# Kernel tuning notes

Measured on AMD Instinct MI355X. Metric: run time of the kernel, lower is better.

Reference implementation:

```python
import jax, jax.numpy as jnp
import numpy as np

SEQ, D_IN, D_OUT = 4096, 1024, 1024


def setup_inputs() -> dict:
    key = jax.random.key(0)
    k_emb, k_q, k_k, k_v = jax.random.split(key, 4)
    # torch Linear stores weight as [out, in]; we keep [in, out] for x @ W
    scale = 1.0 / np.sqrt(D_IN)
    return {
        "embeddings": jax.random.normal(k_emb, (SEQ, D_IN), dtype=jnp.float32),
        "w_query": jax.random.uniform(k_q, (D_IN, D_OUT), dtype=jnp.float32, minval=-scale, maxval=scale),
        "w_key": jax.random.uniform(k_k, (D_IN, D_OUT), dtype=jnp.float32, minval=-scale, maxval=scale),
        "w_value": jax.random.uniform(k_v, (D_IN, D_OUT), dtype=jnp.float32, minval=-scale, maxval=scale),
    }


def reference(embeddings, w_query, w_key, w_value):
    # QKV projections (bias=False)
    q = embeddings @ w_query  # [S, D_out]
    k = embeddings @ w_key    # [S, D_out]
    v = embeddings @ w_value  # [S, D_out]
    inv_sqrt_d = 1.0 / jnp.sqrt(jnp.asarray(k.shape[-1], dtype=q.dtype))
    scores = jnp.einsum("sd,td->st", q, k) * inv_sqrt_d  # [S, S]
    weights = jax.nn.softmax(scores, axis=-1)
    return weights @ v  # [S, D_out]
```

## Files before the change

### kernel.cpp

```cpp
#include <hip/hip_runtime.h>
#include <hip/hip_bf16.h>

typedef unsigned short u16;
typedef __bf16 bf16x8 __attribute__((ext_vector_type(8)));
typedef float f32x4 __attribute__((ext_vector_type(4)));
typedef unsigned short u16x8 __attribute__((ext_vector_type(8)));
typedef unsigned short u16x4 __attribute__((ext_vector_type(4)));

__device__ __forceinline__ float bf2f(u16 u) {
  unsigned x = ((unsigned)u) << 16;
  return __builtin_bit_cast(float, x);
}
__device__ __forceinline__ u16 f2bf(float f) {
  unsigned u = __builtin_bit_cast(unsigned, f);
  u += 0x7fffu + ((u >> 16) & 1u);
  return (u16)(u >> 16);
}

__device__ __forceinline__ void gload16(const u16* g, u16* lds) {
  __builtin_amdgcn_global_load_lds(
      (const __attribute__((address_space(1))) void*)g,
      (__attribute__((address_space(3))) void*)lds,
      16, 0, 0);
}

template <int OUT_MODE, int NX, int BK>
__device__ __forceinline__ void gemm_body(
    const u16* __restrict__ A, int lda,
    const u16* __restrict__ B, int ldb,
    void* __restrict__ C, int ldc, int K, float cscale)
{
  __shared__ __align__(16) u16 As[128 * BK];
  __shared__ __align__(16) u16 Bs[128 * BK];

  constexpr int CPR = BK / 8;
  constexpr int RPG = 512 / BK;
  constexpr int IPW = 32 / RPG;

  const int b = blockIdx.x;
  const int by = (b & 7) + 8 * (b / (8 * NX));
  const int bx = (b >> 3) % NX;
  const int m0 = by * 128, n0 = bx * 128;

  const int t = threadIdx.x;
  const int w = t >> 6, l = t & 63;
  const int srow = l / CPR;
  const int lc = l % CPR;
  const int wm = (w >> 1) * 64, wn = (w & 1) * 64;
  const int fr = l & 15;
  const int q = l >> 4;

  f32x4 acc[4][4] = {};

  for (int kt = 0; kt < K; kt += BK) {
    __syncthreads();
#pragma unroll
    for (int j = 0; j < IPW; ++j) {
      const int rr = RPG * (IPW * w + j);
      const int ga = rr + srow;
      const int sch = ((lc ^ (ga & 7))) * 8;
      gload16(A + (size_t)(m0 + ga) * lda + kt + sch, As + rr * BK);
      gload16(B + (size_t)(n0 + ga) * ldb + kt + sch, Bs + rr * BK);
    }
    __syncthreads();

#pragma unroll
    for (int s = 0; s < BK / 32; ++s) {
      const int j = s * 4 + q;
      bf16x8 af[4], bfr[4];
#pragma unroll
      for (int i = 0; i < 4; ++i) {
        const int ra = wm + 16 * i + fr;
        af[i] = *(const bf16x8*)(As + ra * BK + (j ^ (ra & 7)) * 8);
      }
#pragma unroll
      for (int i = 0; i < 4; ++i) {
        const int rb = wn + 16 * i + fr;
        bfr[i] = *(const bf16x8*)(Bs + rb * BK + (j ^ (rb & 7)) * 8);
      }
#pragma unroll
      for (int i = 0; i < 4; ++i)
#pragma unroll
        for (int jj = 0; jj < 4; ++jj)
          acc[i][jj] = __builtin_amdgcn_mfma_f32_16x16x32_bf16(af[i], bfr[jj], acc[i][jj], 0, 0, 0);
    }
  }

  const int er = q * 4;
  const int ec = l & 15;
#pragma unroll
  for (int i = 0; i < 4; ++i)
#pragma unroll
    for (int jj = 0; jj < 4; ++jj)
#pragma unroll
      for (int r = 0; r < 4; ++r) {
        const size_t idx = (size_t)(m0 + wm + 16 * i + er + r) * ldc + (n0 + wn + 16 * jj + ec);
        if (OUT_MODE == 1) ((u16*)C)[idx] = f2bf(acc[i][jj][r] * cscale);
        else               ((float*)C)[idx] = acc[i][jj][r];
      }
}

__global__ __launch_bounds__(256) void gemm_qkv(const u16* __restrict__ A,
                                                const u16* __restrict__ B,
                                                u16* __restrict__ C) {
  gemm_body<1, 24, 64>(A, 1024, B, 1024, C, 3072, 1024, 1.0f);
}
__global__ __launch_bounds__(256) void gemm_score(const u16* __restrict__ QKV,
                                                  u16* __restrict__ S) {
  gemm_body<1, 32, 64>(QKV, 3072, QKV + 1024, 3072, S, 4096, 1024, 0.03125f);
}
__global__ __launch_bounds__(256) void gemm_pv(const u16* __restrict__ S,
                                               const u16* __restrict__ Vt,
                                               float* __restrict__ O) {
  gemm_body<0, 8, 128>(S, 4096, Vt, 4096, O, 1024, 4096, 1.0f);
}

__global__ __launch_bounds__(256) void cast_f32_bf16(const float* __restrict__ in,
                                                     u16* __restrict__ out) {
  const int i = (blockIdx.x * 256 + threadIdx.x) * 4;
  float4 f = *(const float4*)(in + i);
  u16x4 o;
  o.x = f2bf(f.x); o.y = f2bf(f.y); o.z = f2bf(f.z); o.w = f2bf(f.w);
  *(u16x4*)(out + i) = o;
}

__global__ __launch_bounds__(1024) void transpose_w3(
    const float* __restrict__ w0, const float* __restrict__ w1,
    const float* __restrict__ w2, u16* __restrict__ out)
{
  __shared__ u16 tile[32][33];
  const float* in = (blockIdx.z == 0) ? w0 : (blockIdx.z == 1) ? w1 : w2;
  u16* o = out + (size_t)blockIdx.z * 1024 * 1024;
  const int c0 = blockIdx.x * 32, r0 = blockIdx.y * 32;
  const int tx = threadIdx.x, ty = threadIdx.y;
  tile[ty][tx] = f2bf(in[(size_t)(r0 + ty) * 1024 + c0 + tx]);
  __syncthreads();
  o[(size_t)(c0 + ty) * 1024 + r0 + tx] = tile[tx][ty];
}

__global__ __launch_bounds__(1024) void transpose_bf16(
    const u16* __restrict__ in, int ldin, u16* __restrict__ out, int ldout)
{
  __shared__ u16 tile[32][33];
  const int c0 = blockIdx.x * 32, r0 = blockIdx.y * 32;
  const int tx = threadIdx.x, ty = threadIdx.y;
  tile[ty][tx] = in[(size_t)(r0 + ty) * ldin + c0 + tx];
  __syncthreads();
  out[(size_t)(c0 + ty) * ldout + r0 + tx] = tile[tx][ty];
}

__global__ __launch_bounds__(256) void softmax_rows(u16* __restrict__ S) {
  const int N = 4096;
  u16* p = S + (size_t)blockIdx.x * N;
  const int t = threadIdx.x;
  u16x8 u0 = ((const u16x8*)p)[t * 2];
  u16x8 u1 = ((const u16x8*)p)[t * 2 + 1];
  float v[16];
#pragma unroll
  for (int i = 0; i < 8; ++i) v[i] = bf2f(u0[i]);
#pragma unroll
  for (int i = 0; i < 8; ++i) v[8 + i] = bf2f(u1[i]);

  float m = -1e30f;
#pragma unroll
  for (int i = 0; i < 16; ++i) m = fmaxf(m, v[i]);
#pragma unroll
  for (int off = 32; off; off >>= 1) m = fmaxf(m, __shfl_xor(m, off));
  __shared__ float red[8];
  if ((t & 63) == 0) red[t >> 6] = m;
  __syncthreads();
  m = fmaxf(fmaxf(red[0], red[1]), fmaxf(red[2], red[3]));

  float s = 0.f;
#pragma unroll
  for (int i = 0; i < 16; ++i) { v[i] = __expf(v[i] - m); s += v[i]; }
#pragma unroll
  for (int off = 32; off; off >>= 1) s += __shfl_xor(s, off);
  if ((t & 63) == 0) red[4 + (t >> 6)] = s;
  __syncthreads();
  s = (red[4] + red[5]) + (red[6] + red[7]);
  const float inv = 1.0f / s;

  u16x8 o0, o1;
#pragma unroll
  for (int i = 0; i < 8; ++i) o0[i] = f2bf(v[i] * inv);
#pragma unroll
  for (int i = 0; i < 8; ++i) o1[i] = f2bf(v[8 + i] * inv);
  ((u16x8*)p)[t * 2] = o0;
  ((u16x8*)p)[t * 2 + 1] = o1;
}

extern "C" void kernel_launch(void* const* d_in, const int* in_sizes, int n_in,
                              void* d_out, int out_size, void* d_ws, size_t ws_size,
                              hipStream_t stream) {
  const float* E  = (const float*)d_in[0];
  const float* Wq = (const float*)d_in[1];
  const float* Wk = (const float*)d_in[2];
  const float* Wv = (const float*)d_in[3];
  float* Out = (float*)d_out;

  char* w = (char*)d_ws;
  u16* Ebf = (u16*)(w);
  u16* Wt  = (u16*)(w + (size_t)(8u << 20));
  u16* QKV = (u16*)(w + (size_t)(14u << 20));
  u16* Vt  = (u16*)(w + (size_t)(38u << 20));
  u16* S   = (u16*)(w + (size_t)(46u << 20));

  const dim3 tb(32, 32);

  cast_f32_bf16<<<4096, 256, 0, stream>>>(E, Ebf);
  transpose_w3<<<dim3(32, 32, 3), tb, 0, stream>>>(Wq, Wk, Wv, Wt);

  gemm_qkv<<<768, 256, 0, stream>>>(Ebf, Wt, QKV);

  transpose_bf16<<<dim3(32, 128), tb, 0, stream>>>(QKV + 2048, 3072, Vt, 4096);

  gemm_score<<<1024, 256, 0, stream>>>(QKV, S);

  softmax_rows<<<4096, 256, 0, stream>>>(S);

  gemm_pv<<<256, 256, 0, stream>>>(S, Vt, Out);
}
```

Baseline: 237.1 us.

## Split-K the PV GEMM into two halves and add a reduction pass

The PV GEMM launched only 256 blocks with K=4096. It now splits K into two halves over blockIdx.z, which doubles the block count to fill more compute units. One partial result is written to the output and the other to a workspace buffer that reuses the Ebf region, and a new reduce_add kernel sums them. The cost is an extra 16 MB of fp32 writes and reads plus one more kernel launch.

```diff
diff --git a/kernel.cpp b/kernel.cpp
--- a/kernel.cpp
+++ b/kernel.cpp
@@ -28,7 +28,7 @@
 __device__ __forceinline__ void gemm_body(
     const u16* __restrict__ A, int lda,
     const u16* __restrict__ B, int ldb,
-    void* __restrict__ C, int ldc, int K, float cscale)
+    void* __restrict__ C, int ldc, int kt0, int Kc, float cscale)
 {
   __shared__ __align__(16) u16 As[128 * BK];
   __shared__ __align__(16) u16 Bs[128 * BK];
@@ -52,7 +52,8 @@
 
   f32x4 acc[4][4] = {};
 
-  for (int kt = 0; kt < K; kt += BK) {
+  for (int kk = 0; kk < Kc; kk += BK) {
+    const int kt = kt0 + kk;
     __syncthreads();
 #pragma unroll
     for (int j = 0; j < IPW; ++j) {
@@ -103,16 +104,25 @@
 __global__ __launch_bounds__(256) void gemm_qkv(const u16* __restrict__ A,
                                                 const u16* __restrict__ B,
                                                 u16* __restrict__ C) {
-  gemm_body<1, 24, 64>(A, 1024, B, 1024, C, 3072, 1024, 1.0f);
+  gemm_body<1, 24, 64>(A, 1024, B, 1024, C, 3072, 0, 1024, 1.0f);
 }
 __global__ __launch_bounds__(256) void gemm_score(const u16* __restrict__ QKV,
                                                   u16* __restrict__ S) {
-  gemm_body<1, 32, 64>(QKV, 3072, QKV + 1024, 3072, S, 4096, 1024, 0.03125f);
+  gemm_body<1, 32, 64>(QKV, 3072, QKV + 1024, 3072, S, 4096, 0, 1024, 0.03125f);
 }
 __global__ __launch_bounds__(256) void gemm_pv(const u16* __restrict__ S,
                                                const u16* __restrict__ Vt,
-                                               float* __restrict__ O) {
-  gemm_body<0, 8, 128>(S, 4096, Vt, 4096, O, 1024, 4096, 1.0f);
+                                               float* __restrict__ O0,
+                                               float* __restrict__ O1) {
+  float* C = blockIdx.z ? O1 : O0;
+  gemm_body<0, 8, 128>(S, 4096, Vt, 4096, C, 1024, blockIdx.z * 2048, 2048, 1.0f);
+}
+
+__global__ __launch_bounds__(256) void reduce_add(float4* __restrict__ out,
+                                                  const float4* __restrict__ p) {
+  const int i = blockIdx.x * 256 + threadIdx.x;
+  float4 a = out[i], b = p[i];
+  out[i] = float4{a.x + b.x, a.y + b.y, a.z + b.z, a.w + b.w};
 }
 
 __global__ __launch_bounds__(256) void cast_f32_bf16(const float* __restrict__ in,
@@ -205,19 +215,19 @@
   u16* QKV = (u16*)(w + (size_t)(14u << 20));
   u16* Vt  = (u16*)(w + (size_t)(38u << 20));
   u16* S   = (u16*)(w + (size_t)(46u << 20));
-
-  const dim3 tb(32, 32);
+  float* P1 = (float*)(w);
 
   cast_f32_bf16<<<4096, 256, 0, stream>>>(E, Ebf);
-  transpose_w3<<<dim3(32, 32, 3), tb, 0, stream>>>(Wq, Wk, Wv, Wt);
+  transpose_w3<<<dim3(32, 32, 3), dim3(32, 32), 0, stream>>>(Wq, Wk, Wv, Wt);
 
   gemm_qkv<<<768, 256, 0, stream>>>(Ebf, Wt, QKV);
 
-  transpose_bf16<<<dim3(32, 128), tb, 0, stream>>>(QKV + 2048, 3072, Vt, 4096);
+  transpose_bf16<<<dim3(32, 128), dim3(32, 32), 0, stream>>>(QKV + 2048, 3072, Vt, 4096);
 
   gemm_score<<<1024, 256, 0, stream>>>(QKV, S);
 
   softmax_rows<<<4096, 256, 0, stream>>>(S);
 
-  gemm_pv<<<256, 256, 0, stream>>>(S, Vt, Out);
-}
+  gemm_pv<<<dim3(256, 1, 2), 256, 0, stream>>>(S, Vt, Out, P1);
+  reduce_add<<<4096, 256, 0, stream>>>((float4*)Out, (const float4*)P1);
+}
```

Measured after the change: 223.3 us. 5.8% less time.
